# Kernel optimization log

Measured on AMD Instinct MI355X. Metric: run time of the kernel, lower is better.

The kernel has to match this reference:

```python
import jax, jax.numpy as jnp
import numpy as np

N_STEPS_OUT = 64


def _lstm(x, W, U, b, act):
    """Keras-style LSTM (gate order i,f,c,o). x: [B,T,F] -> h_seq [B,T,units]."""
    xW = jnp.einsum('btf,fg->btg', x, W) + b  # precompute input projections [B,T,4U]

    def step(carry, xt):
        h, c = carry
        z = xt + h @ U
        i, f, g, o = jnp.split(z, 4, axis=-1)
        c = jax.nn.sigmoid(f) * c + jax.nn.sigmoid(i) * act(g)
        h = jax.nn.sigmoid(o) * act(c)
        return (h, c), h

    B = x.shape[0]
    units = U.shape[0]
    init = (jnp.zeros((B, units), x.dtype), jnp.zeros((B, units), x.dtype))
    _, hs = jax.lax.scan(step, init, jnp.swapaxes(xW, 0, 1))
    return jnp.swapaxes(hs, 0, 1)  # [B,T,units]


def setup_inputs() -> dict:
    key = jax.random.key(0)
    ks = jax.random.split(key, 8)
    B, T_in, F = 256, 256, 64
    U_enc, U_dec, F_out = 512, 256, 16
    s = 0.05  # keep gates away from saturation
    return {
        'inputs': jax.random.normal(ks[0], (B, T_in, F), jnp.float32),
        'enc_kernel': jax.random.normal(ks[1], (F, 4 * U_enc), jnp.float32) * s,
        'enc_rec': jax.random.normal(ks[2], (U_enc, 4 * U_enc), jnp.float32) * s,
        'enc_bias': jnp.zeros((4 * U_enc,), jnp.float32),
        'dec_f_kernel': jax.random.normal(ks[3], (U_enc, 4 * U_dec), jnp.float32) * s,
        'dec_f_rec': jax.random.normal(ks[4], (U_dec, 4 * U_dec), jnp.float32) * s,
        'dec_f_bias': jnp.zeros((4 * U_dec,), jnp.float32),
        'dec_b_kernel': jax.random.normal(ks[5], (U_enc, 4 * U_dec), jnp.float32) * s,
        'dec_b_rec': jax.random.normal(ks[6], (U_dec, 4 * U_dec), jnp.float32) * s,
        'dec_b_bias': jnp.zeros((4 * U_dec,), jnp.float32),
        'dense_kernel': jax.random.normal(ks[7], (2 * U_dec, F_out), jnp.float32) * s,
        'dense_bias': jnp.zeros((F_out,), jnp.float32),
    }


def reference(inputs, enc_kernel, enc_rec, enc_bias,
              dec_f_kernel, dec_f_rec, dec_f_bias,
              dec_b_kernel, dec_b_rec, dec_b_bias,
              dense_kernel, dense_bias):
    softmax_act = lambda z: jax.nn.softmax(z, axis=-1)  # non-default LSTM activation
    # Encoder LSTM (activation='softmax'), take last hidden state
    enc_h = _lstm(inputs, enc_kernel, enc_rec, enc_bias, softmax_act)[:, -1, :]  # [B,512]
    # RepeatVector(n_steps_out); dropout is identity at inference
    B, U = enc_h.shape
    rep = jnp.broadcast_to(enc_h[:, None, :], (B, N_STEPS_OUT, U))
    # Bidirectional LSTM(256, return_sequences=True), default tanh activation, concat merge
    fwd = _lstm(rep, dec_f_kernel, dec_f_rec, dec_f_bias, jnp.tanh)
    bwd = _lstm(rep[:, ::-1, :], dec_b_kernel, dec_b_rec, dec_b_bias, jnp.tanh)[:, ::-1, :]
    dec = jnp.concatenate([fwd, bwd], axis=-1)  # [B,T_out,512]
    # TimeDistributed Dense(n_features_out)
    return dec @ dense_kernel + dense_bias
```

## Files before the change

kernel.cpp:

```cpp
#include <hip/hip_runtime.h>
#include <math.h>


typedef __attribute__((ext_vector_type(8))) short bf16x8;
typedef __attribute__((ext_vector_type(8))) unsigned short u16x8;
typedef __attribute__((ext_vector_type(4))) float f32x4;

#define OFS_XW     0u
#define OFS_HEH    524288u
#define OFS_HEL    589824u
#define OFS_HD     655360u
#define OFS_HSEQ   917504u
#define OFS_BENCH  5111808u
#define OFS_BENCL  5701632u
#define OFS_BDKH   6291456u
#define OFS_BDKL   6815744u
#define OFS_BDUH   7340032u
#define OFS_BDUL   7602176u
#define OFS_PST    7864320u
#define OFS_BAR    7897088u
#define WS_FLOATS  7962624u

__device__ __forceinline__ unsigned short bf_hi(float f) {
    union { float f; unsigned u; } v; v.f = f;
    unsigned r = v.u + 0x7fffu + ((v.u >> 16) & 1u);
    return (unsigned short)(r >> 16);
}
__device__ __forceinline__ float bf2f(unsigned short h) {
    union { unsigned u; float f; } v; v.u = ((unsigned)h) << 16;
    return v.f;
}
__device__ __forceinline__ void split2(float f, unsigned short& hi, unsigned short& lo) {
    hi = bf_hi(f);
    lo = bf_hi(f - bf2f(hi));
}
__device__ __forceinline__ float sigm(float x) { return 1.0f / (1.0f + __expf(-x)); }

__device__ __forceinline__ void gspin(unsigned* arr, unsigned tgt, int nslots) {
    const int lane = threadIdx.x & 63;
    const int idx = (lane < nslots) ? lane : 0;
    const long long t0 = clock64();
    for (;;) {
        unsigned v = __hip_atomic_load(arr + idx * 32, __ATOMIC_RELAXED,
                                       __HIP_MEMORY_SCOPE_AGENT);
        #pragma unroll
        for (int m = 32; m; m >>= 1) {
            const unsigned o = (unsigned)__shfl_xor((int)v, m, 64);
            v = (o < v) ? o : v;
        }
        if (v >= tgt) break;
        __builtin_amdgcn_s_sleep(1);
        if (clock64() - t0 > 4000000LL) break;
    }
    asm volatile("buffer_inv sc0" ::: "memory");
}

#define HB(cnt, tgt) do { \
    asm volatile("s_waitcnt vmcnt(0) lgkmcnt(0)" ::: "memory"); \
    if ((threadIdx.x & 63) == 0) atomicAdd((cnt), 1u); \
    const long long _hb0 = clock64(); \
    while (__hip_atomic_load((cnt), __ATOMIC_RELAXED, \
                             __HIP_MEMORY_SCOPE_WORKGROUP) < (tgt)) { \
        __builtin_amdgcn_s_sleep(0); \
        if (clock64() - _hb0 > 8000000LL) break; } \
    asm volatile("" ::: "memory"); } while (0)

#define LDS_SPIN(ptr, tgt) do { \
    const long long _ls0 = clock64(); \
    while (__hip_atomic_load((ptr), __ATOMIC_RELAXED, \
                             __HIP_MEMORY_SCOPE_WORKGROUP) < (tgt)) { \
        __builtin_amdgcn_s_sleep(0); \
        if (clock64() - _ls0 > 8000000LL) break; } \
    asm volatile("" ::: "memory"); } while (0)

__device__ __forceinline__ void arrive_pub(unsigned* arr, int slot, unsigned val) {
    asm volatile("s_waitcnt vmcnt(0) lgkmcnt(0)" ::: "memory");
    __syncthreads();
    if (threadIdx.x == 0)
        __hip_atomic_store(arr + slot * 32, val, __ATOMIC_RELAXED,
                           __HIP_MEMORY_SCOPE_AGENT);
}
__device__ __forceinline__ void wait_min(unsigned* arr, unsigned tgt, int nslots) {
    if (threadIdx.x < 64) gspin(arr, tgt, nslots);
    __syncthreads();
}

__device__ __forceinline__ float red16max(float v) {
    #pragma unroll
    for (int m = 8; m; m >>= 1) v = fmaxf(v, __shfl_xor(v, m, 64));
    return v;
}
__device__ __forceinline__ float red16sum(float v) {
    #pragma unroll
    for (int m = 8; m; m >>= 1) v += __shfl_xor(v, m, 64);
    return v;
}

template <int MODE>
__global__ __launch_bounds__(256) void pack_b(
    const float* __restrict__ S0, const float* __restrict__ S1,
    unsigned short* __restrict__ H, unsigned short* __restrict__ L,
    unsigned* __restrict__ bar)
{
    const int idx = blockIdx.x * 256 + threadIdx.x;
    if (MODE == 0 && idx < 65536) bar[idx] = 0u;
    const int n = idx & 2047, kg = idx >> 11;
    int sc;
    const float* Sd;
    if (MODE == 0) {
        sc = ((n >> 4) & 3) * 512 + (n >> 6) * 16 + (n & 15);
        Sd = nullptr;
    } else {
        const int dir = n >> 10, bw = (n >> 6) & 15;
        sc = ((n >> 4) & 3) * 256 + bw * 16 + (n & 15);
        Sd = dir ? S1 : S0;
    }
    u16x8 h8, l8;
    #pragma unroll
    for (int j = 0; j < 8; ++j) {
        const int k = kg * 8 + j;
        float v;
        if (MODE == 0) v = (k < 64) ? S0[(size_t)k * 2048 + sc] : S1[(size_t)(k - 64) * 2048 + sc];
        else           v = Sd[(size_t)k * 1024 + sc];
        unsigned short hh, ll; split2(v, hh, ll);
        h8[j] = hh; l8[j] = ll;
    }
    *(u16x8*)(H + (size_t)idx * 8) = h8;
    *(u16x8*)(L + (size_t)idx * 8) = l8;
}

__global__ __launch_bounds__(512, 2) void lstm_all(
    const float* __restrict__ x, const float* __restrict__ encB,
    const float* __restrict__ dfB, const float* __restrict__ dbB,
    const float* __restrict__ dK, const float* __restrict__ dnB,
    float* __restrict__ out, float* __restrict__ ws)
{
    const int bid = blockIdx.x, tid = threadIdx.x;
    const int g = bid & 7, w = bid >> 3;
    const int lane = tid & 63, wid = tid >> 6;
    const int half = wid >> 2, gate = wid & 3;
    const int l16 = lane >> 4, lr = lane & 15;
    const int lrow = half * 16 + lr;
    const int grow = g * 32 + lrow;
    const int ncl  = gate * 16 + lr;
    const int gcolp = w * 64 + ncl;
    const int tidh = tid & 255;
    const int urh = tidh >> 4, ul = tidh & 15;
    const int urow = half * 16 + urh;

    float* xw = ws + OFS_XW;
    unsigned short* hEHu = (unsigned short*)(ws + OFS_HEH);
    unsigned short* hELu = (unsigned short*)(ws + OFS_HEL);
    unsigned short* hseqb = (unsigned short*)(ws + OFS_HSEQ);
    const unsigned short* BeH = (const unsigned short*)(ws + OFS_BENCH);
    const unsigned short* BeL = (const unsigned short*)(ws + OFS_BENCL);
    const unsigned short* BkH = (const unsigned short*)(ws + OFS_BDKH);
    const unsigned short* BkL = (const unsigned short*)(ws + OFS_BDKL);
    const unsigned short* BuH = (const unsigned short*)(ws + OFS_BDUH);
    const unsigned short* BuL = (const unsigned short*)(ws + OFS_BDUL);
    float* pst1 = ws + OFS_PST + (unsigned)g * 2048u;
    float* pst2 = ws + OFS_PST + 16384u + (unsigned)g * 2048u;
    unsigned* barg = (unsigned*)(ws + OFS_BAR) + g * 8192;
    unsigned* pC = barg;
    unsigned* pAh[2] = {barg + 1024, barg + 2048};
    unsigned* pBh[2] = {barg + 3072, barg + 4096};
    unsigned* pE = barg + 6144;

    __shared__ __align__(16) unsigned short sBe[32768];
    __shared__ __align__(16) float zt[2112];
    __shared__ float scl[32];
    __shared__ unsigned harr[2], hrel[2];

    const int dir = w >> 4, bw = w & 15;
    unsigned* pD = barg + 5120 + dir * 512;
    unsigned short* hd[2][2];
    #pragma unroll
    for (int p = 0; p < 2; ++p)
        #pragma unroll
        for (int hl_ = 0; hl_ < 2; ++hl_)
            hd[p][hl_] = (unsigned short*)(ws + OFS_HD +
                          (unsigned)((p * 2 + dir) * 2 + hl_) * 32768u);

    if (tid < 2) { harr[tid] = 0u; hrel[tid] = 0u; }

    {
        const int urow32 = tid >> 4, ul32 = tid & 15;
        const int u = w * 16 + ul32;
        const size_t he = ((size_t)(g * 64 + (u >> 3)) * 32 + urow32) * 8 + (u & 7);
        hEHu[he] = 0; hELu[he] = 0;
        const size_t hdix = (size_t)(g * 32 + urow32) * 256 + bw * 16 + ul32;
        #pragma unroll
        for (int p = 0; p < 2; ++p) { hd[p][0][hdix] = 0; hd[p][1][hdix] = 0; }
        if (ul32 == 0) *(float2*)(pst2 + (urow32 * 32 + w) * 2) = float2{0.f, 1.f};
    }
    for (int i = tid; i < 4096; i += 512) {
        const int kg8 = i >> 6, nc = i & 63;
        *(u16x8*)(sBe + i * 8) =
            *(const u16x8*)(BeH + ((size_t)(kg8 + 8) * 2048 + w * 64 + nc) * 8);
    }
    arrive_pub(pC, w, 1u);

    const float encBias = encB[gate * 512 + w * 16 + lr];
    float c = 0.f;

    for (int t = 0; t < 256; ++t) {
        f32x4 ax = {0.f, 0.f, 0.f, 0.f};
        #pragma unroll
        for (int kw = 0; kw < 2; ++kw) {
            const int kg = kw * 4 + l16;
            const float* xp = x + (size_t)grow * 16384 + t * 64 + kg * 8;
            const float4 x0 = *(const float4*)xp;
            const float4 x1 = *(const float4*)(xp + 4);
            const float xs[8] = {x0.x, x0.y, x0.z, x0.w, x1.x, x1.y, x1.z, x1.w};
            bf16x8 a_h, a_l;
            #pragma unroll
            for (int j = 0; j < 8; ++j) {
                unsigned short hh, ll; split2(xs[j], hh, ll);
                a_h[j] = (short)hh; a_l[j] = (short)ll;
            }
            const size_t bo = ((size_t)kg * 2048 + gcolp) * 8;
            const bf16x8 b_h = *(const bf16x8*)(BeH + bo);
            const bf16x8 b_l = *(const bf16x8*)(BeL + bo);
            ax = __builtin_amdgcn_mfma_f32_16x16x32_bf16(a_h, b_h, ax, 0, 0, 0);
            ax = __builtin_amdgcn_mfma_f32_16x16x32_bf16(a_h, b_l, ax, 0, 0, 0);
            ax = __builtin_amdgcn_mfma_f32_16x16x32_bf16(a_l, b_h, ax, 0, 0, 0);
        }
        if (gate == 0) {
            if (t == 0) gspin(pC, 1u, 32);
            else        gspin(pBh[half], (unsigned)t, 32);
            if (lane == 0) atomicAdd(&hrel[half], 1u);
        }
        LDS_SPIN(&hrel[half], (unsigned)(2 * t + 1));

        {
            const float2 pa = *(const float2*)(pst2 + (urow * 32 + ul) * 2);
            const float2 pb = *(const float2*)(pst2 + (urow * 32 + ul + 16) * 2);
            const float ml = fmaxf(pa.x, pb.x);
            const float sl = pa.y * __expf(pa.x - ml) + pb.y * __expf(pb.x - ml);
            const float M2 = red16max(ml);
            const float S2 = red16sum(sl * __expf(ml - M2));
            if (ul == 0) scl[urow] = __expf(-M2) / S2;
        }
        HB(&harr[half], 4u * (4 * t + 1));

        f32x4 ah = {0.f, 0.f, 0.f, 0.f};
        #pragma unroll
        for (int kw = 2; kw < 18; ++kw) {
            const int kg = kw * 4 + l16;
            const size_t ao = ((size_t)(g * 64 + (kg - 8)) * 32 + lrow) * 8;
            const bf16x8 a_h = *(const bf16x8*)(hEHu + ao);
            const bf16x8 a_l = *(const bf16x8*)(hELu + ao);
            const bf16x8 b_h = *(const bf16x8*)(sBe + ((kg - 8) * 64 + ncl) * 8);
            const bf16x8 b_l = *(const bf16x8*)(BeL + ((size_t)kg * 2048 + gcolp) * 8);
            ah = __builtin_amdgcn_mfma_f32_16x16x32_bf16(a_h, b_h, ah, 0, 0, 0);
            ah = __builtin_amdgcn_mfma_f32_16x16x32_bf16(a_h, b_l, ah, 0, 0, 0);
            ah = __builtin_amdgcn_mfma_f32_16x16x32_bf16(a_l, b_h, ah, 0, 0, 0);
        }
        #pragma unroll
        for (int r = 0; r < 4; ++r) {
            const int row = half * 16 + l16 * 4 + r;
            zt[ncl * 33 + row] = scl[row] * ah[r] + ax[r] + encBias;
        }
        HB(&harr[half], 4u * (4 * t + 2));

        const float zg = zt[(32 + ul) * 33 + urow];
        {
            const float mw = red16max(zg);
            const float sw = red16sum(__expf(zg - mw));
            if (ul == 0) *(float2*)(pst1 + (urow * 32 + w) * 2) = float2{mw, sw};
        }
        const float si = sigm(zt[ul * 33 + urow]);
        const float sf = sigm(zt[(16 + ul) * 33 + urow]);
        const float so = sigm(zt[(48 + ul) * 33 + urow]);
        HB(&harr[half], 4u * (4 * t + 3));

        if (gate == 0) {
            if (lane == 0)
                __hip_atomic_store(pAh[half] + w * 32, (unsigned)(t + 1),
                                   __ATOMIC_RELAXED, __HIP_MEMORY_SCOPE_AGENT);
            gspin(pAh[half], (unsigned)(t + 1), 32);
            if (lane == 0) atomicAdd(&hrel[half], 1u);
        }
        LDS_SPIN(&hrel[half], (unsigned)(2 * t + 2));

        {
            const float2 pa = *(const float2*)(pst1 + (urow * 32 + ul) * 2);
            const float2 pb = *(const float2*)(pst1 + (urow * 32 + ul + 16) * 2);
            const float ml = fmaxf(pa.x, pb.x);
            const float sl = pa.y * __expf(pa.x - ml) + pb.y * __expf(pb.x - ml);
            const float M = red16max(ml);
            const float S = red16sum(sl * __expf(ml - M));
            c = sf * c + si * (__expf(zg - M) / S);
        }
        {
            const float ht = so * __expf(c);
            unsigned short hh, hl; split2(ht, hh, hl);
            const int u = w * 16 + ul;
            const size_t he = ((size_t)(g * 64 + (u >> 3)) * 32 + urow) * 8 + (u & 7);
            hEHu[he] = hh;
            hELu[he] = hl;
            const float m2 = red16max(c);
            const float s2 = red16sum(__expf(c - m2));
            if (ul == 0) *(float2*)(pst2 + (urow * 32 + w) * 2) = float2{m2, s2};
        }
        HB(&harr[half], 4u * (4 * t + 4));
        if (gate == 0 && lane == 0)
            __hip_atomic_store(pBh[half] + w * 32, (unsigned)(t + 1),
                               __ATOMIC_RELAXED, __HIP_MEMORY_SCOPE_AGENT);
    }

    __syncthreads();
    wait_min(pBh[0], 256u, 32);
    wait_min(pBh[1], 256u, 32);

    {
        const int urow32 = tid >> 4, ul32 = tid & 15;
        const float2 pa = *(const float2*)(pst2 + (urow32 * 32 + ul32) * 2);
        const float2 pb = *(const float2*)(pst2 + (urow32 * 32 + ul32 + 16) * 2);
        const float ml = fmaxf(pa.x, pb.x);
        const float sl = pa.y * __expf(pa.x - ml) + pb.y * __expf(pb.x - ml);
        const float M2 = red16max(ml);
        const float S2 = red16sum(sl * __expf(ml - M2));
        if (ul32 == 0) scl[urow32] = __expf(-M2) / S2;
    }
    __syncthreads();
    const int dmh = wid & 1, dnh = wid >> 1;
    const int dlrow = dmh * 16 + lr;
    const int dncl = dnh * 16 + lr;
    const int dgcolp = w * 64 + dncl;
    {
        const float bias = (dir ? dbB : dfB)[dnh * 256 + bw * 16 + lr];
        f32x4 acc = {0.f, 0.f, 0.f, 0.f};
        #pragma unroll
        for (int kw = 0; kw < 16; ++kw) {
            const int kg = kw * 4 + l16;
            const size_t ao = ((size_t)(g * 64 + kg) * 32 + dlrow) * 8;
            const bf16x8 a_h = *(const bf16x8*)(hEHu + ao);
            const bf16x8 a_l = *(const bf16x8*)(hELu + ao);
            const size_t bo = ((size_t)kg * 2048 + dgcolp) * 8;
            const bf16x8 b_h = *(const bf16x8*)(BkH + bo);
            const bf16x8 b_l = *(const bf16x8*)(BkL + bo);
            acc = __builtin_amdgcn_mfma_f32_16x16x32_bf16(a_h, b_h, acc, 0, 0, 0);
            acc = __builtin_amdgcn_mfma_f32_16x16x32_bf16(a_h, b_l, acc, 0, 0, 0);
            acc = __builtin_amdgcn_mfma_f32_16x16x32_bf16(a_l, b_h, acc, 0, 0, 0);
        }
        float* xp = xw + (size_t)(g * 32 + dmh * 16 + l16 * 4) * 2048 + dgcolp;
        #pragma unroll
        for (int r = 0; r < 4; ++r) {
            const int prow = dmh * 16 + l16 * 4 + r;
            xp[2048 * r] = scl[prow] * acc[r] + bias;
        }
    }
    asm volatile("s_waitcnt vmcnt(0)" ::: "memory");
    __syncthreads();

    for (int i = tid; i < 2048; i += 512) {
        const int kg = i >> 6, nc = i & 63;
        *(u16x8*)(sBe + i * 8) =
            *(const u16x8*)(BuH + ((size_t)kg * 2048 + w * 64 + nc) * 8);
    }
    __syncthreads();

    float cd = 0.f;
    const int durow = tid >> 4, dul = tid & 15;
    const float* xr = xw + (size_t)(g * 32 + durow) * 2048 + w * 64;
    for (int s = 0; s < 64; ++s) {
        if (s) { arrive_pub(pD, bw, (unsigned)s); wait_min(pD, (unsigned)s, 16); }
        const int par = s & 1;
        f32x4 acc = {0.f, 0.f, 0.f, 0.f};
        #pragma unroll
        for (int kw = 0; kw < 8; ++kw) {
            const int kg = kw * 4 + l16;
            const size_t ao = (size_t)(g * 32 + dlrow) * 256 + (size_t)kg * 8;
            const bf16x8 a_h = *(const bf16x8*)(hd[par][0] + ao);
            const bf16x8 a_l = *(const bf16x8*)(hd[par][1] + ao);
            const bf16x8 b_h = *(const bf16x8*)(sBe + (kg * 64 + dncl) * 8);
            const bf16x8 b_l = *(const bf16x8*)(BuL + ((size_t)kg * 2048 + dgcolp) * 8);
            acc = __builtin_amdgcn_mfma_f32_16x16x32_bf16(a_h, b_h, acc, 0, 0, 0);
            acc = __builtin_amdgcn_mfma_f32_16x16x32_bf16(a_h, b_l, acc, 0, 0, 0);
            acc = __builtin_amdgcn_mfma_f32_16x16x32_bf16(a_l, b_h, acc, 0, 0, 0);
        }
        #pragma unroll
        for (int r = 0; r < 4; ++r)
            zt[dncl * 33 + dmh * 16 + l16 * 4 + r] = acc[r];
        __syncthreads();
        {
            const float zi = zt[dul * 33 + durow]        + xr[dul];
            const float zf = zt[(16 + dul) * 33 + durow] + xr[16 + dul];
            const float zg = zt[(32 + dul) * 33 + durow] + xr[32 + dul];
            const float zo = zt[(48 + dul) * 33 + durow] + xr[48 + dul];
            const float cv = sigm(zf) * cd + sigm(zi) * tanhf(zg);
            cd = cv;
            const float hv = sigm(zo) * tanhf(cv);
            unsigned short hh, hl; split2(hv, hh, hl);
            const size_t hdix = (size_t)(g * 32 + durow) * 256 + bw * 16 + dul;
            hd[par ^ 1][0][hdix] = hh;
            hd[par ^ 1][1][hdix] = hl;
            const int tt = dir ? (63 - s) : s;
            hseqb[((size_t)(g * 32 + durow) * 64 + tt) * 512 + dir * 256 + bw * 16 + dul] = hh;
        }
        __syncthreads();
    }
    arrive_pub(pE, w, 1u); wait_min(pE, 1u, 32);

    {
        float* dkc = (float*)sBe;
        for (int i = tid; i < 8192; i += 512) dkc[i] = dK[i];
        __syncthreads();
        const int f = tid & 15;
        #pragma unroll
        for (int p = 0; p < 2; ++p) {
            const int bt = g * 2048 + w * 64 + (tid >> 4) + p * 32;
            const unsigned short* hs = hseqb + (size_t)bt * 512;
            float acc = dnB[f];
            #pragma unroll 4
            for (int k = 0; k < 512; k += 8) {
                const u16x8 hv = *(const u16x8*)(hs + k);
                #pragma unroll
                for (int j = 0; j < 8; ++j)
                    acc += bf2f(hv[j]) * dkc[(k + j) * 16 + f];
            }
            out[(size_t)bt * 16 + f] = acc;
        }
    }
}

extern "C" void kernel_launch(void* const* d_in, const int* in_sizes, int n_in,
                              void* d_out, int out_size, void* d_ws, size_t ws_size,
                              hipStream_t stream)
{
    const float* x    = (const float*)d_in[0];
    const float* encW = (const float*)d_in[1];
    const float* encU = (const float*)d_in[2];
    const float* encB = (const float*)d_in[3];
    const float* dfK  = (const float*)d_in[4];
    const float* dfU  = (const float*)d_in[5];
    const float* dfB  = (const float*)d_in[6];
    const float* dbK  = (const float*)d_in[7];
    const float* dbU  = (const float*)d_in[8];
    const float* dbB  = (const float*)d_in[9];
    const float* dK   = (const float*)d_in[10];
    const float* dnB  = (const float*)d_in[11];

    if (ws_size < WS_FLOATS * sizeof(float)) return;

    float* ws = (float*)d_ws;
    unsigned short* BencH = (unsigned short*)(ws + OFS_BENCH);
    unsigned short* BencL = (unsigned short*)(ws + OFS_BENCL);
    unsigned short* BdkH  = (unsigned short*)(ws + OFS_BDKH);
    unsigned short* BdkL  = (unsigned short*)(ws + OFS_BDKL);
    unsigned short* BduH  = (unsigned short*)(ws + OFS_BDUH);
    unsigned short* BduL  = (unsigned short*)(ws + OFS_BDUL);
    unsigned* bar = (unsigned*)(ws + OFS_BAR);

    pack_b<0><<<576, 256, 0, stream>>>(encW, encU, BencH, BencL, bar);
    pack_b<1><<<512, 256, 0, stream>>>(dfK, dbK, BdkH, BdkL, nullptr);
    pack_b<2><<<256, 256, 0, stream>>>(dfU, dbU, BduH, BduL, nullptr);

    lstm_all<<<256, 512, 0, stream>>>(x, encB, dfB, dbB, dK, dnB,
                                      (float*)d_out, ws);
}
```

Measured before the change: 2.619 ms.

## Cache all encoder and decoder weight halves in LDS and drop one per-step barrier

Both the bf16 high and low halves of the encoder input and recurrent weights (and the decoder recurrent weights) are now held in shared memory, so the per-step MFMA operands no longer come from global memory. This needs about 147KB of LDS, so launch bounds drop to one block per CU. The softmax partial max/sum for the g gate is computed directly from the MFMA accumulators by the gate-2 waves, and their publish flag is set there. That removes one block-level barrier per timestep and starts the cross-block exchange earlier. The trade-off is lower occupancy and a somewhat longer per-step critical path in the gate-2 waves.

```diff
diff --git a/kernel.cpp b/kernel.cpp
--- a/kernel.cpp
+++ b/kernel.cpp
@@ -129,7 +129,7 @@
     *(u16x8*)(L + (size_t)idx * 8) = l8;
 }
 
-__global__ __launch_bounds__(512, 2) void lstm_all(
+__global__ __launch_bounds__(512, 1) void lstm_all(
     const float* __restrict__ x, const float* __restrict__ encB,
     const float* __restrict__ dfB, const float* __restrict__ dbB,
     const float* __restrict__ dK, const float* __restrict__ dnB,
@@ -143,7 +143,6 @@
     const int lrow = half * 16 + lr;
     const int grow = g * 32 + lrow;
     const int ncl  = gate * 16 + lr;
-    const int gcolp = w * 64 + ncl;
     const int tidh = tid & 255;
     const int urh = tidh >> 4, ul = tidh & 15;
     const int urow = half * 16 + urh;
@@ -166,7 +165,8 @@
     unsigned* pBh[2] = {barg + 3072, barg + 4096};
     unsigned* pE = barg + 6144;
 
-    __shared__ __align__(16) unsigned short sBe[32768];
+    __shared__ __align__(16) unsigned short sBeH[36864];
+    __shared__ __align__(16) unsigned short sBeL[36864];
     __shared__ __align__(16) float zt[2112];
     __shared__ float scl[32];
     __shared__ unsigned harr[2], hrel[2];
@@ -193,10 +193,11 @@
         for (int p = 0; p < 2; ++p) { hd[p][0][hdix] = 0; hd[p][1][hdix] = 0; }
         if (ul32 == 0) *(float2*)(pst2 + (urow32 * 32 + w) * 2) = float2{0.f, 1.f};
     }
-    for (int i = tid; i < 4096; i += 512) {
-        const int kg8 = i >> 6, nc = i & 63;
-        *(u16x8*)(sBe + i * 8) =
-            *(const u16x8*)(BeH + ((size_t)(kg8 + 8) * 2048 + w * 64 + nc) * 8);
+    for (int i = tid; i < 4608; i += 512) {
+        const int kg = i >> 6, nc = i & 63;
+        const size_t src = ((size_t)kg * 2048 + w * 64 + nc) * 8;
+        *(u16x8*)(sBeH + i * 8) = *(const u16x8*)(BeH + src);
+        *(u16x8*)(sBeL + i * 8) = *(const u16x8*)(BeL + src);
     }
     arrive_pub(pC, w, 1u);
 
@@ -218,9 +219,8 @@
                 unsigned short hh, ll; split2(xs[j], hh, ll);
                 a_h[j] = (short)hh; a_l[j] = (short)ll;
             }
-            const size_t bo = ((size_t)kg * 2048 + gcolp) * 8;
-            const bf16x8 b_h = *(const bf16x8*)(BeH + bo);
-            const bf16x8 b_l = *(const bf16x8*)(BeL + bo);
+            const bf16x8 b_h = *(const bf16x8*)(sBeH + (kg * 64 + ncl) * 8);
+            const bf16x8 b_l = *(const bf16x8*)(sBeL + (kg * 64 + ncl) * 8);
             ax = __builtin_amdgcn_mfma_f32_16x16x32_bf16(a_h, b_h, ax, 0, 0, 0);
             ax = __builtin_amdgcn_mfma_f32_16x16x32_bf16(a_h, b_l, ax, 0, 0, 0);
             ax = __builtin_amdgcn_mfma_f32_16x16x32_bf16(a_l, b_h, ax, 0, 0, 0);
@@ -241,7 +241,7 @@
             const float S2 = red16sum(sl * __expf(ml - M2));
             if (ul == 0) scl[urow] = __expf(-M2) / S2;
         }
-        HB(&harr[half], 4u * (4 * t + 1));
+        HB(&harr[half], 4u * (3 * t + 1));
 
         f32x4 ah = {0.f, 0.f, 0.f, 0.f};
         #pragma unroll
@@ -250,34 +250,44 @@
             const size_t ao = ((size_t)(g * 64 + (kg - 8)) * 32 + lrow) * 8;
             const bf16x8 a_h = *(const bf16x8*)(hEHu + ao);
             const bf16x8 a_l = *(const bf16x8*)(hELu + ao);
-            const bf16x8 b_h = *(const bf16x8*)(sBe + ((kg - 8) * 64 + ncl) * 8);
-            const bf16x8 b_l = *(const bf16x8*)(BeL + ((size_t)kg * 2048 + gcolp) * 8);
+            const bf16x8 b_h = *(const bf16x8*)(sBeH + (kg * 64 + ncl) * 8);
+            const bf16x8 b_l = *(const bf16x8*)(sBeL + (kg * 64 + ncl) * 8);
             ah = __builtin_amdgcn_mfma_f32_16x16x32_bf16(a_h, b_h, ah, 0, 0, 0);
             ah = __builtin_amdgcn_mfma_f32_16x16x32_bf16(a_h, b_l, ah, 0, 0, 0);
             ah = __builtin_amdgcn_mfma_f32_16x16x32_bf16(a_l, b_h, ah, 0, 0, 0);
         }
+        float v[4];
         #pragma unroll
         for (int r = 0; r < 4; ++r) {
             const int row = half * 16 + l16 * 4 + r;
-            zt[ncl * 33 + row] = scl[row] * ah[r] + ax[r] + encBias;
-        }
-        HB(&harr[half], 4u * (4 * t + 2));
+            v[r] = scl[row] * ah[r] + ax[r] + encBias;
+        }
+        if (gate == 2) {
+            #pragma unroll
+            for (int r = 0; r < 4; ++r) {
+                const float mw = red16max(v[r]);
+                const float sw = red16sum(__expf(v[r] - mw));
+                if (lr == 0) {
+                    const int row = half * 16 + l16 * 4 + r;
+                    *(float2*)(pst1 + (row * 32 + w) * 2) = float2{mw, sw};
+                }
+            }
+            asm volatile("s_waitcnt vmcnt(0)" ::: "memory");
+            if (lane == 0)
+                __hip_atomic_store(pAh[half] + w * 32, (unsigned)(t + 1),
+                                   __ATOMIC_RELAXED, __HIP_MEMORY_SCOPE_AGENT);
+        }
+        #pragma unroll
+        for (int r = 0; r < 4; ++r)
+            zt[ncl * 33 + half * 16 + l16 * 4 + r] = v[r];
+        HB(&harr[half], 4u * (3 * t + 2));
 
         const float zg = zt[(32 + ul) * 33 + urow];
-        {
-            const float mw = red16max(zg);
-            const float sw = red16sum(__expf(zg - mw));
-            if (ul == 0) *(float2*)(pst1 + (urow * 32 + w) * 2) = float2{mw, sw};
-        }
         const float si = sigm(zt[ul * 33 + urow]);
         const float sf = sigm(zt[(16 + ul) * 33 + urow]);
         const float so = sigm(zt[(48 + ul) * 33 + urow]);
-        HB(&harr[half], 4u * (4 * t + 3));
 
         if (gate == 0) {
-            if (lane == 0)
-                __hip_atomic_store(pAh[half] + w * 32, (unsigned)(t + 1),
-                                   __ATOMIC_RELAXED, __HIP_MEMORY_SCOPE_AGENT);
             gspin(pAh[half], (unsigned)(t + 1), 32);
             if (lane == 0) atomicAdd(&hrel[half], 1u);
         }
@@ -303,7 +313,7 @@
             const float s2 = red16sum(__expf(c - m2));
             if (ul == 0) *(float2*)(pst2 + (urow * 32 + w) * 2) = float2{m2, s2};
         }
-        HB(&harr[half], 4u * (4 * t + 4));
+        HB(&harr[half], 4u * (3 * t + 3));
         if (gate == 0 && lane == 0)
             __hip_atomic_store(pBh[half] + w * 32, (unsigned)(t + 1),
                                __ATOMIC_RELAXED, __HIP_MEMORY_SCOPE_AGENT);
@@ -356,8 +366,9 @@
 
     for (int i = tid; i < 2048; i += 512) {
         const int kg = i >> 6, nc = i & 63;
-        *(u16x8*)(sBe + i * 8) =
-            *(const u16x8*)(BuH + ((size_t)kg * 2048 + w * 64 + nc) * 8);
+        const size_t src = ((size_t)kg * 2048 + w * 64 + nc) * 8;
+        *(u16x8*)(sBeH + i * 8) = *(const u16x8*)(BuH + src);
+        *(u16x8*)(sBeL + i * 8) = *(const u16x8*)(BuL + src);
     }
     __syncthreads();
 
@@ -374,8 +385,8 @@
             const size_t ao = (size_t)(g * 32 + dlrow) * 256 + (size_t)kg * 8;
             const bf16x8 a_h = *(const bf16x8*)(hd[par][0] + ao);
             const bf16x8 a_l = *(const bf16x8*)(hd[par][1] + ao);
-            const bf16x8 b_h = *(const bf16x8*)(sBe + (kg * 64 + dncl) * 8);
-            const bf16x8 b_l = *(const bf16x8*)(BuL + ((size_t)kg * 2048 + dgcolp) * 8);
+            const bf16x8 b_h = *(const bf16x8*)(sBeH + (kg * 64 + dncl) * 8);
+            const bf16x8 b_l = *(const bf16x8*)(sBeL + (kg * 64 + dncl) * 8);
             acc = __builtin_amdgcn_mfma_f32_16x16x32_bf16(a_h, b_h, acc, 0, 0, 0);
             acc = __builtin_amdgcn_mfma_f32_16x16x32_bf16(a_h, b_l, acc, 0, 0, 0);
             acc = __builtin_amdgcn_mfma_f32_16x16x32_bf16(a_l, b_h, acc, 0, 0, 0);
@@ -404,7 +415,7 @@
     arrive_pub(pE, w, 1u); wait_min(pE, 1u, 32);
 
     {
-        float* dkc = (float*)sBe;
+        float* dkc = (float*)sBeH;
         for (int i = tid; i < 8192; i += 512) dkc[i] = dK[i];
         __syncthreads();
         const int f = tid & 15;
```

After: 2.346 ms. -10.4%, faster.
